# Kernel tuning notes

Measured on AMD Instinct MI355X. Metric: run time of the kernel, lower is better.

## Reference

```python
import jax, jax.numpy as jnp
import numpy as np

DIM = 1024; DEPTH = 6; HEADS = 16; DH = 64; NF = 16; VOCAB = 20000; B = 4; N = 1024
INNER = HEADS * DH
FF_INNER = int(DIM * 4 * 2 / 3)  # GEGLU inner dim = 2730


def _ln(x, g):
    # torch F.layer_norm with beta=0 buffer, eps=1e-5
    m = x.mean(-1, keepdims=True)
    v = ((x - m) ** 2).mean(-1, keepdims=True)
    return (x - m) / jnp.sqrt(v + 1e-5) * g


def _attn(x, ctx, mask, ln_g, Wq, Wkv, Wo):
    # faithful: LayerNorm applied to x (queries); context, if given, used raw for k/v
    xn = _ln(x, ln_g)
    kv_x = xn if ctx is None else ctx
    b, i, _ = x.shape
    j = kv_x.shape[1]
    q = (xn @ Wq).reshape(b, i, HEADS, DH) * (DH ** -0.5)
    k, v = jnp.split(kv_x @ Wkv, 2, axis=-1)
    k = k.reshape(b, j, HEADS, DH)
    v = v.reshape(b, j, HEADS, DH)
    sim = jnp.einsum('bihd,bjhd->bhij', q, k)
    sim = jnp.where(mask, sim, -jnp.finfo(sim.dtype).max)
    attn = jax.nn.softmax(sim, axis=-1)
    out = jnp.einsum('bhij,bjhd->bihd', attn, v).reshape(b, i, INNER)
    return out @ Wo


def _closs(a, b, ls):
    # CLIP-style ContrastiveLossWithTemperature
    an = a / jnp.linalg.norm(a, axis=-1, keepdims=True)
    bn = b / jnp.linalg.norm(b, axis=-1, keepdims=True)
    logits = jnp.exp(ls) * (an @ bn.T)
    lab = jnp.arange(a.shape[0])
    la = -jax.nn.log_softmax(logits, axis=-1)[lab, lab].mean()
    lb = -jax.nn.log_softmax(logits.T, axis=-1)[lab, lab].mean()
    return (la + lb) * 0.5


def setup_inputs() -> dict:
    key = jax.random.key(0)
    ks = jax.random.split(key, 16)
    rn = lambda k, s: jax.random.normal(k, s, jnp.float32) * 0.02
    return {
        'spliced_data': jax.random.normal(ks[0], (B, N), jnp.float32),
        'spliced_index': jax.random.randint(ks[1], (B, N), 0, VOCAB),
        'emb': rn(ks[2], (VOCAB, DIM)),
        'fusion_tokens': jax.random.normal(ks[3], (NF, DIM), jnp.float32),
        'return_tokens': jax.random.normal(ks[4], (2, DIM), jnp.float32),
        'ln1_g': jnp.ones((DEPTH, DIM), jnp.float32),
        'Wq': rn(ks[5], (DEPTH, DIM, INNER)),
        'Wkv': rn(ks[6], (DEPTH, DIM, 2 * INNER)),
        'Wo': rn(ks[7], (DEPTH, INNER, DIM)),
        'ln2_g': jnp.ones((DEPTH, DIM), jnp.float32),
        'Wff1': rn(ks[8], (DEPTH, DIM, 2 * FF_INNER)),
        'Wff2': rn(ks[9], (DEPTH, FF_INNER, DIM)),
        'norm_g': jnp.ones((DIM,), jnp.float32),
        'pool_ln_g': jnp.ones((DIM,), jnp.float32),
        'pWq': rn(ks[10], (DIM, INNER)),
        'pWkv': rn(ks[11], (DIM, 2 * INNER)),
        'pWo': rn(ks[12], (INNER, DIM)),
        'logit_scale_c': jnp.float32(np.log(1.0 / 0.07)),
        'logit_scale_f': jnp.float32(np.log(1.0 / 0.07)),
    }


def reference(spliced_data, spliced_index, emb, fusion_tokens, return_tokens,
              ln1_g, Wq, Wkv, Wo, ln2_g, Wff1, Wff2, norm_g,
              pool_ln_g, pWq, pWkv, pWo, logit_scale_c, logit_scale_f):
    b = spliced_data.shape[0]
    # BioZorroEncoder: value-weighted embedding lookup
    spliced_tokens = emb[spliced_index] * spliced_data[..., None]  # [b, N, DIM]
    tokens = jnp.concatenate(
        [spliced_tokens, jnp.broadcast_to(fusion_tokens, (b, NF, DIM))], axis=1)
    tt = jnp.concatenate([jnp.zeros((N,), jnp.int32), jnp.ones((NF,), jnp.int32)])
    # spliced attends spliced; fusion attends everything
    zmask = (tt[:, None] == tt[None, :]) | (tt[:, None] == 1)

    def body(t, p):
        l1, wq, wkv, wo, l2, w1, w2 = p
        t = _attn(t, None, zmask, l1, wq, wkv, wo) + t
        h = _ln(t, l2) @ w1
        xh, gate = jnp.split(h, 2, axis=-1)
        t = (jax.nn.gelu(gate, approximate=False) * xh) @ w2 + t
        return t, None

    tokens, _ = jax.lax.scan(body, tokens, (ln1_g, Wq, Wkv, Wo, ln2_g, Wff1, Wff2))
    tokens = _ln(tokens, norm_g)

    rtt = jnp.array([0, 1], jnp.int32)
    pm0 = rtt[:, None] == tt[None, :]
    # faithful to source operator precedence: (pm0 | rtt) == GLOBAL(2) -> all False
    pm = (pm0.astype(jnp.int32) | rtt[:, None]) == 2

    ret = jnp.broadcast_to(return_tokens, (b, 2, DIM))
    pooled = _attn(ret, tokens, pm, pool_ln_g, pWq, pWkv, pWo) + ret

    spliced = pooled[:, 0]
    fusion = pooled[:, 1]
    loss = _closs(spliced, spliced, logit_scale_c) + _closs(spliced, fusion, logit_scale_f)
    return loss
```

## Files before the change

### kernel.cpp

```cpp
#include <hip/hip_runtime.h>

typedef unsigned short u16;
typedef unsigned long long u64;
typedef __attribute__((ext_vector_type(8))) short short8;
typedef __attribute__((ext_vector_type(4))) float f32x4;

__device__ __forceinline__ u16 f2b(float f) {
  union { float f; unsigned u; } x; x.f = f;
  unsigned r = x.u + 0x7fffu + ((x.u >> 16) & 1u);
  return (u16)(r >> 16);
}
__device__ __forceinline__ float b2f(u16 h) {
  union { unsigned u; float f; } x; x.u = ((unsigned)h) << 16;
  return x.f;
}
__device__ __forceinline__ void gld16(const void* g, void* l) {
  __builtin_amdgcn_global_load_lds(
      (__attribute__((address_space(1))) const void*)g,
      (__attribute__((address_space(3))) void*)l, 16, 0, 0);
}

__global__ __launch_bounds__(256) void embed_k(
    const float* __restrict__ data, const int* __restrict__ idx,
    const float* __restrict__ emb, const float* __restrict__ fus,
    float* __restrict__ t) {
  int row = blockIdx.x;
  int b = row / 1040, n = row % 1040;
  int tid = threadIdx.x;
  const float4* src;
  float sc = 1.f;
  if (n < 1024) {
    int e = idx[b * 1024 + n];
    sc = data[b * 1024 + n];
    src = (const float4*)(emb + (long)e * 1024);
  } else {
    src = (const float4*)(fus + (long)(n - 1024) * 1024);
  }
  float4 v = src[tid];
  v.x *= sc; v.y *= sc; v.z *= sc; v.w *= sc;
  ((float4*)(t + (long)row * 1024))[tid] = v;
}

__global__ __launch_bounds__(256) void wtrans5_k(
    const float* __restrict__ sWq, const float* __restrict__ sWkv,
    const float* __restrict__ sWo, const float* __restrict__ sW1,
    const float* __restrict__ sW2,
    u16* __restrict__ dQkvT, u16* __restrict__ dWoT,
    u16* __restrict__ dF1T, u16* __restrict__ dF2T) {
  int id = blockIdx.x;
  const float* src; u16* dst; int K, N, Kpad, nx; float sc = 1.f;
  if (id < 1024)       { src = sWq;  dst = dQkvT;             K = 1024; N = 1024; Kpad = 1024; nx = 32; sc = 0.125f; }
  else if (id < 3072)  { id -= 1024; src = sWkv; dst = dQkvT + 1024 * 1024; K = 1024; N = 2048; Kpad = 1024; nx = 64; }
  else if (id < 4096)  { id -= 3072; src = sWo;  dst = dWoT;  K = 1024; N = 1024; Kpad = 1024; nx = 32; }
  else if (id < 9600)  { id -= 4096; src = sW1;  dst = dF1T;  K = 1024; N = 5460; Kpad = 1024; nx = 172; }
  else                 { id -= 9600; src = sW2;  dst = dF2T;  K = 2730; N = 1024; Kpad = 2752; nx = 32; }
  int n0 = (id % nx) * 32, k0 = (id / nx) * 32;
  __shared__ float tile[32][33];
  int x = threadIdx.x & 31, y = threadIdx.x >> 5;
#pragma unroll
  for (int i = 0; i < 4; i++) {
    int k = k0 + y + i * 8, n = n0 + x;
    tile[y + i * 8][x] = (k < K && n < N) ? src[(long)k * N + n] * sc : 0.f;
  }
  __syncthreads();
#pragma unroll
  for (int i = 0; i < 4; i++) {
    int n = n0 + y + i * 8, k = k0 + x;
    dst[(long)n * Kpad + k] = f2b(tile[x][y + i * 8]);
  }
}

__global__ __launch_bounds__(256) void ln_k(
    const float* __restrict__ t, const float* __restrict__ g,
    u16* __restrict__ xn) {
  int row = blockIdx.x, tid = threadIdx.x;
  int wave = tid >> 6, lane = tid & 63;
  float4 v = ((const float4*)(t + (long)row * 1024))[tid];
  float s = v.x + v.y + v.z + v.w;
#pragma unroll
  for (int o = 32; o > 0; o >>= 1) s += __shfl_xor(s, o, 64);
  __shared__ float r1[4], r2[4];
  if (lane == 0) r1[wave] = s;
  __syncthreads();
  float mean = (r1[0] + r1[1] + r1[2] + r1[3]) * (1.f / 1024.f);
  float dx = v.x - mean, dy = v.y - mean, dz = v.z - mean, dw = v.w - mean;
  float q = dx * dx + dy * dy + dz * dz + dw * dw;
#pragma unroll
  for (int o = 32; o > 0; o >>= 1) q += __shfl_xor(q, o, 64);
  if (lane == 0) r2[wave] = q;
  __syncthreads();
  float var = (r2[0] + r2[1] + r2[2] + r2[3]) * (1.f / 1024.f);
  float inv = rsqrtf(var + 1e-5f);
  float4 gv = ((const float4*)g)[tid];
  u64 pack = (u64)f2b(dx * inv * gv.x)
           | ((u64)f2b(dy * inv * gv.y) << 16)
           | ((u64)f2b(dz * inv * gv.z) << 32)
           | ((u64)f2b(dw * inv * gv.w) << 48);
  *(u64*)(xn + (long)row * 1024 + tid * 4) = pack;
}

__global__ __launch_bounds__(256) void lnred_k(
    float* __restrict__ t, const float* __restrict__ p0, const float* __restrict__ p1,
    const float* __restrict__ g, u16* __restrict__ xn) {
  int row = blockIdx.x, tid = threadIdx.x;
  int wave = tid >> 6, lane = tid & 63;
  long base = (long)row * 1024;
  float4 v = ((const float4*)(t + base))[tid];
  float4 a = ((const float4*)(p0 + base))[tid];
  float4 bq = ((const float4*)(p1 + base))[tid];
  v.x += a.x + bq.x; v.y += a.y + bq.y; v.z += a.z + bq.z; v.w += a.w + bq.w;
  ((float4*)(t + base))[tid] = v;
  float s = v.x + v.y + v.z + v.w;
#pragma unroll
  for (int o = 32; o > 0; o >>= 1) s += __shfl_xor(s, o, 64);
  __shared__ float r1[4], r2[4];
  if (lane == 0) r1[wave] = s;
  __syncthreads();
  float mean = (r1[0] + r1[1] + r1[2] + r1[3]) * (1.f / 1024.f);
  float dx = v.x - mean, dy = v.y - mean, dz = v.z - mean, dw = v.w - mean;
  float q = dx * dx + dy * dy + dz * dz + dw * dw;
#pragma unroll
  for (int o = 32; o > 0; o >>= 1) q += __shfl_xor(q, o, 64);
  if (lane == 0) r2[wave] = q;
  __syncthreads();
  float var = (r2[0] + r2[1] + r2[2] + r2[3]) * (1.f / 1024.f);
  float inv = rsqrtf(var + 1e-5f);
  float4 gv = ((const float4*)g)[tid];
  u64 pack = (u64)f2b(dx * inv * gv.x)
           | ((u64)f2b(dy * inv * gv.y) << 16)
           | ((u64)f2b(dz * inv * gv.z) << 32)
           | ((u64)f2b(dw * inv * gv.w) << 48);
  *(u64*)(xn + base + tid * 4) = pack;
}

__global__ __launch_bounds__(256) void redrow_k(
    float* __restrict__ t, const float* __restrict__ p0, const float* __restrict__ p1,
    float* __restrict__ rowm, float* __restrict__ rinv) {
  int row = blockIdx.x, tid = threadIdx.x;
  int wave = tid >> 6, lane = tid & 63;
  long base = (long)row * 1024;
  float4 v = ((const float4*)(t + base))[tid];
  float4 a = ((const float4*)(p0 + base))[tid];
  float4 bq = ((const float4*)(p1 + base))[tid];
  v.x += a.x + bq.x; v.y += a.y + bq.y; v.z += a.z + bq.z; v.w += a.w + bq.w;
  ((float4*)(t + base))[tid] = v;
  float s = v.x + v.y + v.z + v.w;
#pragma unroll
  for (int o = 32; o > 0; o >>= 1) s += __shfl_xor(s, o, 64);
  __shared__ float r1[4], r2[4];
  if (lane == 0) r1[wave] = s;
  __syncthreads();
  float mean = (r1[0] + r1[1] + r1[2] + r1[3]) * (1.f / 1024.f);
  float dx = v.x - mean, dy = v.y - mean, dz = v.z - mean, dw = v.w - mean;
  float q = dx * dx + dy * dy + dz * dz + dw * dw;
#pragma unroll
  for (int o = 32; o > 0; o >>= 1) q += __shfl_xor(q, o, 64);
  if (lane == 0) r2[wave] = q;
  __syncthreads();
  if (tid == 0) {
    float var = (r2[0] + r2[1] + r2[2] + r2[3]) * (1.f / 1024.f);
    rowm[row] = mean;
    rinv[row] = rsqrtf(var + 1e-5f);
  }
}

__global__ __launch_bounds__(256) void gemm_bt(
    const u16* __restrict__ A, int lda,
    const u16* __restrict__ Bt, int ldb,
    void* __restrict__ C, int ldc,
    int K, int mode, int gx, int ns, long pstride, u16* __restrict__ vt) {
  __shared__ u16 As[3][128 * 32];
  __shared__ u16 Bs[3][128 * 32];
  int tid = threadIdx.x;
  int wave = tid >> 6, lane = tid & 63;
  int col = lane & 15, grp = lane >> 4;
  int nwg = gridDim.x;
  int id = blockIdx.x;
  int q = nwg >> 3, r = nwg & 7;
  int xcd = id & 7, off = id >> 3;
  int wgid = (xcd < r ? xcd * (q + 1) : r * (q + 1) + (xcd - r) * q) + off;
  int tiles = nwg / ns;
  int ksp = wgid / tiles;
  int rem = wgid % tiles;
  int bm = rem % gx, bn = rem / gx;
  int nst = K >> 5;
  int k0 = ((nst * ksp) / ns) << 5;
  int k1 = ((nst * (ksp + 1)) / ns) << 5;
  int sr = wave * 16 + (lane >> 2);
  int sk = ((lane & 3) ^ ((lane >> 3) & 3)) * 8;
  const u16* aSrc = A + ((long)bm * 128 + sr) * lda + sk;
  const u16* bSrc = Bt + ((long)bn * 128 + sr) * ldb + sk;
  int wm = (wave >> 1) * 64, wn = (wave & 1) * 64;
  f32x4 acc[4][4] = {};

#define GSTAGE(buf, kt) do { \
    _Pragma("unroll") \
    for (int qq = 0; qq < 2; qq++) { \
      gld16(aSrc + (kt) + (long)qq * 64 * lda, &As[buf][wave * 512 + qq * 2048]); \
      gld16(bSrc + (kt) + (long)qq * 64 * ldb, &Bs[buf][wave * 512 + qq * 2048]); \
    } } while (0)

  GSTAGE(0, k0);
  if (k0 + 32 < k1) GSTAGE(1, k0 + 32);
  int cur = 0;
  int slot = (grp ^ ((col >> 1) & 3)) * 8;
  for (int kt = k0; kt < k1; kt += 32) {
    if (kt + 64 < k1) {
      int nb = cur + 2; if (nb >= 3) nb -= 3;
      GSTAGE(nb, kt + 64);
      asm volatile("s_waitcnt vmcnt(8)" ::: "memory");
    } else if (kt + 32 < k1) {
      asm volatile("s_waitcnt vmcnt(4)" ::: "memory");
    } else {
      asm volatile("s_waitcnt vmcnt(0)" ::: "memory");
    }
    __builtin_amdgcn_s_barrier();
    __builtin_amdgcn_sched_barrier(0);
    short8 af[4], bfv[4];
#pragma unroll
    for (int m = 0; m < 4; m++)
      af[m] = *(const short8*)&As[cur][(wm + m * 16 + col) * 32 + slot];
#pragma unroll
    for (int n = 0; n < 4; n++)
      bfv[n] = *(const short8*)&Bs[cur][(wn + n * 16 + col) * 32 + slot];
    __builtin_amdgcn_s_setprio(1);
#pragma unroll
    for (int m = 0; m < 4; m++)
#pragma unroll
      for (int n = 0; n < 4; n++)
        acc[m][n] = __builtin_amdgcn_mfma_f32_16x16x32_bf16(af[m], bfv[n], acc[m][n], 0, 0, 0);
    __builtin_amdgcn_s_setprio(0);
    __builtin_amdgcn_s_barrier();
    __builtin_amdgcn_sched_barrier(0);
    cur = (cur == 2) ? 0 : cur + 1;
  }
#undef GSTAGE
  long r0 = (long)bm * 128 + wm + grp * 4;
  int c0 = bn * 128 + wn + col;
  if (mode != 1) {
    u16* Cb = (u16*)C;
#pragma unroll
    for (int m = 0; m < 4; m++)
#pragma unroll
      for (int n = 0; n < 4; n++)
#pragma unroll
        for (int rr = 0; rr < 4; rr++)
          Cb[(r0 + m * 16 + rr) * ldc + c0 + n * 16] = f2b(acc[m][n][rr]);
    if (mode == 2 && bn >= 16) {
#pragma unroll
      for (int m = 0; m < 4; m++) {
        long row = r0 + m * 16;
        if (row < 4160) {
          int bidx = (int)(row / 1040);
          int j = (int)(row - (long)bidx * 1040);
#pragma unroll
          for (int n = 0; n < 4; n++) {
            int d = c0 + n * 16 - 2048;
            u64 pack = (u64)f2b(acc[m][n][0])
                     | ((u64)f2b(acc[m][n][1]) << 16)
                     | ((u64)f2b(acc[m][n][2]) << 32)
                     | ((u64)f2b(acc[m][n][3]) << 48);
            *(u64*)(vt + ((long)(bidx * 16 + (d >> 6)) * 64 + (d & 63)) * 1040 + j) = pack;
          }
        }
      }
    }
  } else {
    float* Cf = (float*)C + (long)ksp * pstride;
#pragma unroll
    for (int m = 0; m < 4; m++)
#pragma unroll
      for (int n = 0; n < 4; n++)
#pragma unroll
        for (int rr = 0; rr < 4; rr++)
          Cf[(r0 + m * 16 + rr) * ldc + c0 + n * 16] = acc[m][n][rr];
  }
}

__global__ __launch_bounds__(256) void attn_k(
    const u16* __restrict__ qkv, const u16* __restrict__ vt,
    u16* __restrict__ out) {
  int bh = blockIdx.x, it = blockIdx.y;
  int b = bh >> 4, h = bh & 15;
  int tid = threadIdx.x, wave = tid >> 6, lane = tid & 63;
  int col = lane & 15, grp = lane >> 4;
  int i0 = it * 64;
  int jmax = (it == 16) ? 1040 : 1024;
  const u16* qb = qkv + (long)b * 1040 * 3072 + h * 64;
  const u16* kb = qkv + (long)b * 1040 * 3072 + 1024 + h * 64;
  const u16* vb = vt + (long)bh * 64 * 1040;
  __shared__ u16 Ks[2][64 * 64];
  __shared__ u16 Vs[2][64 * 64];
  __shared__ u16 Ps[4][16 * 64];

  int srow0 = wave * 8 + (lane >> 3);
  int gsw = ((lane & 7) ^ (srow0 & 7)) * 8;
#define ASTAGE(buf, j0s) do { \
    int jv = (j0s) + gsw; if (jv >= 1040) jv = 1032; \
    _Pragma("unroll") \
    for (int qq = 0; qq < 2; qq++) { \
      int rr = qq * 32 + srow0; \
      gld16(kb + (long)((j0s) + rr) * 3072 + gsw, &Ks[buf][qq * 2048 + wave * 512]); \
      gld16(vb + (long)rr * 1040 + jv, &Vs[buf][qq * 2048 + wave * 512]); \
    } } while (0)

  short8 aq[2];
  int qrow = i0 + wave * 16;
#pragma unroll
  for (int kf = 0; kf < 2; kf++)
    aq[kf] = *(const short8*)(qb + (long)(qrow + col) * 3072 + kf * 32 + grp * 8);

  short8 one8 = {};
  if (col == 0) {
#pragma unroll
    for (int i = 0; i < 8; i++) one8[i] = (short)0x3F80;
  }

  f32x4 oa[4] = {};
  f32x4 oa1 = {};

  ASTAGE(0, 0);
  int cur = 0;
  for (int j0 = 0; j0 < jmax; j0 += 64) {
    if (j0 + 64 < jmax) {
      ASTAGE(cur ^ 1, j0 + 64);
      asm volatile("s_waitcnt vmcnt(4)" ::: "memory");
    } else {
      asm volatile("s_waitcnt vmcnt(0)" ::: "memory");
    }
    __builtin_amdgcn_s_barrier();
    __builtin_amdgcn_sched_barrier(0);
    f32x4 s[4] = {};
#pragma unroll
    for (int kf = 0; kf < 2; kf++) {
      short8 bk[4];
#pragma unroll
      for (int n = 0; n < 4; n++) {
        int rk = n * 16 + col;
        bk[n] = *(const short8*)&Ks[cur][rk * 64 + ((kf * 32 + grp * 8) ^ ((rk & 7) << 3))];
      }
      __builtin_amdgcn_s_setprio(1);
#pragma unroll
      for (int n = 0; n < 4; n++)
        s[n] = __builtin_amdgcn_mfma_f32_16x16x32_bf16(aq[kf], bk[n], s[n], 0, 0, 0);
      __builtin_amdgcn_s_setprio(0);
    }
    if (j0 + 64 > jmax) {
      int lim = jmax - j0;
#pragma unroll
      for (int n = 0; n < 4; n++) {
        if (n * 16 + col >= lim) {
#pragma unroll
          for (int r = 0; r < 4; r++) s[n][r] = -1e30f;
        }
      }
    }
#pragma unroll
    for (int r = 0; r < 4; r++) {
      int rp = grp * 4 + r;
#pragma unroll
      for (int n = 0; n < 4; n++) {
        float p = __expf(s[n][r]);
        Ps[wave][rp * 64 + ((n * 16 + col) ^ ((rp & 7) << 3))] = f2b(p);
      }
    }
#pragma unroll
    for (int kf = 0; kf < 2; kf++) {
      short8 ap, bv[4];
      int rm = col;
      ap = *(const short8*)&Ps[wave][rm * 64 + ((kf * 32 + grp * 8) ^ ((rm & 7) << 3))];
#pragma unroll
      for (int n = 0; n < 4; n++) {
        int rv = n * 16 + col;
        bv[n] = *(const short8*)&Vs[cur][rv * 64 + ((kf * 32 + grp * 8) ^ ((rv & 7) << 3))];
      }
      __builtin_amdgcn_s_setprio(1);
#pragma unroll
      for (int n = 0; n < 4; n++)
        oa[n] = __builtin_amdgcn_mfma_f32_16x16x32_bf16(ap, bv[n], oa[n], 0, 0, 0);
      oa1 = __builtin_amdgcn_mfma_f32_16x16x32_bf16(ap, one8, oa1, 0, 0, 0);
      __builtin_amdgcn_s_setprio(0);
    }
    __builtin_amdgcn_s_barrier();
    __builtin_amdgcn_sched_barrier(0);
    cur ^= 1;
  }
#undef ASTAGE
  float lr[4];
#pragma unroll
  for (int r = 0; r < 4; r++) lr[r] = __shfl(oa1[r], lane & 48, 64);
#pragma unroll
  for (int n = 0; n < 4; n++)
#pragma unroll
    for (int r = 0; r < 4; r++) {
      int i = i0 + wave * 16 + grp * 4 + r;
      if (i < 1040)
        out[((long)b * 1040 + i) * 1024 + h * 64 + n * 16 + col] = f2b(oa[n][r] / lr[r]);
    }
}

__global__ __launch_bounds__(256) void act_k(
    const u16* __restrict__ h, u16* __restrict__ act) {
  int row = blockIdx.x;
  int c = blockIdx.y * 1024 + threadIdx.x * 4;
  if (c >= 2752) return;
  const u16* hr = h + (long)row * 5504;
  u64 pack = 0;
#pragma unroll
  for (int i = 0; i < 4; i++) {
    int cc = c + i;
    float r = 0.f;
    if (cc < 2730) {
      float xh = b2f(hr[cc]);
      float gt = b2f(hr[2730 + cc]);
      float ge = 0.5f * gt * (1.f + erff(gt * 0.70710678118f));
      r = ge * xh;
    }
    pack |= ((u64)f2b(r)) << (16 * i);
  }
  *(u64*)(act + (long)row * 2752 + c) = pack;
}

__global__ __launch_bounds__(256) void wcolsum_k(
    const float* __restrict__ t, const float* __restrict__ rowm,
    const float* __restrict__ rinv, float* __restrict__ colsum,
    float* __restrict__ msum) {
  int b = blockIdx.x, c = blockIdx.y, tid = threadIdx.x;
  float a0 = 0, a1 = 0, a2 = 0, a3 = 0, ms = 0;
  for (int r = 0; r < 20; r++) {
    long row = (long)b * 1040 + c * 20 + r;
    float iv = rinv[row];
    float4 v = ((const float4*)(t + row * 1024))[tid];
    a0 += v.x * iv; a1 += v.y * iv; a2 += v.z * iv; a3 += v.w * iv;
    if (tid == 0) ms += rowm[row] * iv;
  }
  atomicAdd(&colsum[b * 1024 + tid * 4 + 0], a0);
  atomicAdd(&colsum[b * 1024 + tid * 4 + 1], a1);
  atomicAdd(&colsum[b * 1024 + tid * 4 + 2], a2);
  atomicAdd(&colsum[b * 1024 + tid * 4 + 3], a3);
  if (tid == 0) atomicAdd(&msum[b], ms);
}

__global__ __launch_bounds__(256) void mv1_k(
    const float* __restrict__ colsum, const float* __restrict__ msum,
    const float* __restrict__ g, const float* __restrict__ pWkv,
    float* __restrict__ tmp) {
  int b = blockIdx.x, n = blockIdx.y * 256 + threadIdx.x;
  float msb = msum[b];
  float acc = 0.f;
  for (int k = 0; k < 1024; k++) {
    float mk = g[k] * (colsum[b * 1024 + k] - msb);
    acc += mk * pWkv[(long)k * 2048 + 1024 + n];
  }
  tmp[b * 1024 + n] = acc * (1.f / 1040.f);
}

__global__ __launch_bounds__(256) void mv2_k(
    const float* __restrict__ tmp, const float* __restrict__ pWo,
    const float* __restrict__ ret, float* __restrict__ spl,
    float* __restrict__ fub) {
  int b = blockIdx.x, n = blockIdx.y * 256 + threadIdx.x;
  float acc = 0.f;
  for (int k = 0; k < 1024; k++) acc += tmp[b * 1024 + k] * pWo[(long)k * 1024 + n];
  spl[b * 1024 + n] = ret[n] + acc;
  fub[b * 1024 + n] = ret[1024 + n] + acc;
}

__device__ float closs_dev(const float L[4][4]) {
  float la = 0.f, lb = 0.f;
  for (int i = 0; i < 4; i++) {
    float mx = fmaxf(fmaxf(L[i][0], L[i][1]), fmaxf(L[i][2], L[i][3]));
    float sm = expf(L[i][0] - mx) + expf(L[i][1] - mx) + expf(L[i][2] - mx) + expf(L[i][3] - mx);
    la += mx + logf(sm) - L[i][i];
  }
  for (int j = 0; j < 4; j++) {
    float mx = fmaxf(fmaxf(L[0][j], L[1][j]), fmaxf(L[2][j], L[3][j]));
    float sm = expf(L[0][j] - mx) + expf(L[1][j] - mx) + expf(L[2][j] - mx) + expf(L[3][j] - mx);
    lb += mx + logf(sm) - L[j][j];
  }
  return 0.125f * (la + lb);
}

__global__ __launch_bounds__(256) void loss_k(
    const float* __restrict__ s, const float* __restrict__ f,
    const float* __restrict__ lsc, const float* __restrict__ lsf,
    float* __restrict__ out) {
  __shared__ float dots[36];
  int tid = threadIdx.x, wave = tid >> 6, lane = tid & 63;
  for (int d = wave; d < 36; d += 4) {
    const float *a, *bb;
    if (d < 16) { a = s + (d >> 2) * 1024; bb = s + (d & 3) * 1024; }
    else if (d < 32) { int e = d - 16; a = s + (e >> 2) * 1024; bb = f + (e & 3) * 1024; }
    else { a = f + (d - 32) * 1024; bb = a; }
    float p = 0.f;
    for (int k = lane; k < 1024; k += 64) p += a[k] * bb[k];
#pragma unroll
    for (int o = 32; o > 0; o >>= 1) p += __shfl_xor(p, o, 64);
    if (lane == 0) dots[d] = p;
  }
  __syncthreads();
  if (tid == 0) {
    float nS[4], nF[4];
    for (int i = 0; i < 4; i++) { nS[i] = sqrtf(dots[i * 4 + i]); nF[i] = sqrtf(dots[32 + i]); }
    float e1 = expf(lsc[0]), e2 = expf(lsf[0]);
    float L1[4][4], L2[4][4];
    for (int i = 0; i < 4; i++)
      for (int j = 0; j < 4; j++) {
        L1[i][j] = e1 * dots[i * 4 + j] / (nS[i] * nS[j]);
        L2[i][j] = e2 * dots[16 + i * 4 + j] / (nS[i] * nF[j]);
      }
    out[0] = closs_dev(L1) + closs_dev(L2);
  }
}

extern "C" void kernel_launch(void* const* d_in, const int* in_sizes, int n_in,
                              void* d_out, int out_size, void* d_ws, size_t ws_size,
                              hipStream_t stream) {
  (void)in_sizes; (void)n_in; (void)out_size; (void)ws_size;
  const float* sdata = (const float*)d_in[0];
  const int*   sidx  = (const int*)d_in[1];
  const float* emb   = (const float*)d_in[2];
  const float* fus   = (const float*)d_in[3];
  const float* ret   = (const float*)d_in[4];
  const float* ln1g  = (const float*)d_in[5];
  const float* Wq    = (const float*)d_in[6];
  const float* Wkv   = (const float*)d_in[7];
  const float* Wo    = (const float*)d_in[8];
  const float* ln2g  = (const float*)d_in[9];
  const float* Wff1  = (const float*)d_in[10];
  const float* Wff2  = (const float*)d_in[11];
  const float* normg = (const float*)d_in[12];
  const float* pWkv  = (const float*)d_in[15];
  const float* pWo   = (const float*)d_in[16];
  const float* lsc   = (const float*)d_in[17];
  const float* lsf   = (const float*)d_in[18];

  char* ws = (char*)d_ws;
  float* t   = (float*)(ws + 0L);
  u16* xn    = (u16*)(ws + 17301504L);
  char* U    = ws + 25952256L;
  u16* qkv   = (u16*)(U);
  u16* vtb   = (u16*)(U + 26738688L);
  u16* aout  = (u16*)(U + 35270656L);
  u16* hb    = (u16*)(U);
  u16* ab    = (u16*)(U + 46497792L);
  float* par0 = (float*)(U);
  float* par1 = (float*)(U + 17301504L);
  char* WT   = ws + 95698944L;
  u16* qkvT  = (u16*)(WT);
  u16* WoT   = (u16*)(WT + 6291456L);
  u16* f1T   = (u16*)(WT + 8388608L);
  u16* f2T   = (u16*)(WT + 19660800L);
  char* FIN  = ws + 120995840L;
  float* rowm   = (float*)(FIN);
  float* rinvp  = (float*)(FIN + 16640L);
  float* colsum = (float*)(FIN + 33280L);
  float* msum   = (float*)(FIN + 49664L);
  float* tmp    = (float*)(FIN + 49728L);
  float* spl    = (float*)(FIN + 66112L);
  float* fub    = (float*)(FIN + 82496L);
  const long PSTR = 4224L * 1024;

  embed_k<<<4160, 256, 0, stream>>>(sdata, sidx, emb, fus, t);

  for (int l = 0; l < 6; l++) {
    wtrans5_k<<<12352, 256, 0, stream>>>(
        Wq + (long)l * 1024 * 1024, Wkv + (long)l * 1024 * 2048,
        Wo + (long)l * 1024 * 1024, Wff1 + (long)l * 1024 * 5460,
        Wff2 + (long)l * 2730 * 1024, qkvT, WoT, f1T, f2T);

    if (l == 0)
      ln_k<<<4160, 256, 0, stream>>>(t, ln1g, xn);
    else
      lnred_k<<<4160, 256, 0, stream>>>(t, par0, par1, ln1g + l * 1024, xn);

    gemm_bt<<<33 * 24, 256, 0, stream>>>(xn, 1024, qkvT, 1024, qkv, 3072, 1024, 2, 33, 1, 0, vtb);
    attn_k<<<dim3(64, 17), 256, 0, stream>>>(qkv, vtb, aout);
    gemm_bt<<<33 * 8 * 2, 256, 0, stream>>>(aout, 1024, WoT, 1024, par0, 1024, 1024, 1, 33, 2, PSTR, vtb);
    lnred_k<<<4160, 256, 0, stream>>>(t, par0, par1, ln2g + l * 1024, xn);
    gemm_bt<<<33 * 43, 256, 0, stream>>>(xn, 1024, f1T, 1024, hb, 5504, 1024, 0, 33, 1, 0, vtb);
    act_k<<<dim3(4160, 3), 256, 0, stream>>>(hb, ab);
    gemm_bt<<<33 * 8 * 2, 256, 0, stream>>>(ab, 2752, f2T, 2752, par0, 1024, 2752, 1, 33, 2, PSTR, vtb);
  }

  redrow_k<<<4160, 256, 0, stream>>>(t, par0, par1, rowm, rinvp);
  hipMemsetAsync(colsum, 0, 16448, stream);
  wcolsum_k<<<dim3(4, 52), 256, 0, stream>>>(t, rowm, rinvp, colsum, msum);
  mv1_k<<<dim3(4, 4), 256, 0, stream>>>(colsum, msum, normg, pWkv, tmp);
  mv2_k<<<dim3(4, 4), 256, 0, stream>>>(tmp, pWo, ret, spl, fub);
  loss_k<<<1, 256, 0, stream>>>(spl, fub, lsc, lsf, (float*)d_out);
}
```

Measured before the change: 1.993 ms.

## Batch weight transposes into one launch, store split-K partials as bf16, vectorize act loads

Measured after the change: 3.246 ms. 62.9% more time.

```diff
diff --git a/kernel.cpp b/kernel.cpp
--- a/kernel.cpp
+++ b/kernel.cpp
@@ -41,19 +41,20 @@
   ((float4*)(t + (long)row * 1024))[tid] = v;
 }
 
-__global__ __launch_bounds__(256) void wtrans5_k(
+__global__ __launch_bounds__(256) void wtrans6_k(
     const float* __restrict__ sWq, const float* __restrict__ sWkv,
     const float* __restrict__ sWo, const float* __restrict__ sW1,
-    const float* __restrict__ sW2,
-    u16* __restrict__ dQkvT, u16* __restrict__ dWoT,
-    u16* __restrict__ dF1T, u16* __restrict__ dF2T) {
-  int id = blockIdx.x;
+    const float* __restrict__ sW2, u16* __restrict__ wt6) {
+  int gid = blockIdx.x;
+  int l = gid / 12352;
+  int id = gid - l * 12352;
+  u16* base = wt6 + (long)l * 12648448;
   const float* src; u16* dst; int K, N, Kpad, nx; float sc = 1.f;
-  if (id < 1024)       { src = sWq;  dst = dQkvT;             K = 1024; N = 1024; Kpad = 1024; nx = 32; sc = 0.125f; }
-  else if (id < 3072)  { id -= 1024; src = sWkv; dst = dQkvT + 1024 * 1024; K = 1024; N = 2048; Kpad = 1024; nx = 64; }
-  else if (id < 4096)  { id -= 3072; src = sWo;  dst = dWoT;  K = 1024; N = 1024; Kpad = 1024; nx = 32; }
-  else if (id < 9600)  { id -= 4096; src = sW1;  dst = dF1T;  K = 1024; N = 5460; Kpad = 1024; nx = 172; }
-  else                 { id -= 9600; src = sW2;  dst = dF2T;  K = 2730; N = 1024; Kpad = 2752; nx = 32; }
+  if (id < 1024)       { src = sWq  + (long)l * 1048576; dst = base;           K = 1024; N = 1024; Kpad = 1024; nx = 32; sc = 0.125f; }
+  else if (id < 3072)  { id -= 1024; src = sWkv + (long)l * 2097152; dst = base + 1048576; K = 1024; N = 2048; Kpad = 1024; nx = 64; }
+  else if (id < 4096)  { id -= 3072; src = sWo  + (long)l * 1048576; dst = base + 3145728; K = 1024; N = 1024; Kpad = 1024; nx = 32; }
+  else if (id < 9600)  { id -= 4096; src = sW1  + (long)l * 5591040; dst = base + 4194304; K = 1024; N = 5460; Kpad = 1024; nx = 172; }
+  else                 { id -= 9600; src = sW2  + (long)l * 2795520; dst = base + 9830400; K = 2730; N = 1024; Kpad = 2752; nx = 32; }
   int n0 = (id % nx) * 32, k0 = (id / nx) * 32;
   __shared__ float tile[32][33];
   int x = threadIdx.x & 31, y = threadIdx.x >> 5;
@@ -100,15 +101,18 @@
 }
 
 __global__ __launch_bounds__(256) void lnred_k(
-    float* __restrict__ t, const float* __restrict__ p0, const float* __restrict__ p1,
+    float* __restrict__ t, const u16* __restrict__ par, long pstr,
     const float* __restrict__ g, u16* __restrict__ xn) {
   int row = blockIdx.x, tid = threadIdx.x;
   int wave = tid >> 6, lane = tid & 63;
   long base = (long)row * 1024;
   float4 v = ((const float4*)(t + base))[tid];
-  float4 a = ((const float4*)(p0 + base))[tid];
-  float4 bq = ((const float4*)(p1 + base))[tid];
-  v.x += a.x + bq.x; v.y += a.y + bq.y; v.z += a.z + bq.z; v.w += a.w + bq.w;
+  u64 a0 = *(const u64*)(par + base + tid * 4);
+  u64 a1 = *(const u64*)(par + pstr + base + tid * 4);
+  v.x += b2f((u16)a0) + b2f((u16)a1);
+  v.y += b2f((u16)(a0 >> 16)) + b2f((u16)(a1 >> 16));
+  v.z += b2f((u16)(a0 >> 32)) + b2f((u16)(a1 >> 32));
+  v.w += b2f((u16)(a0 >> 48)) + b2f((u16)(a1 >> 48));
   ((float4*)(t + base))[tid] = v;
   float s = v.x + v.y + v.z + v.w;
 #pragma unroll
@@ -134,15 +138,18 @@
 }
 
 __global__ __launch_bounds__(256) void redrow_k(
-    float* __restrict__ t, const float* __restrict__ p0, const float* __restrict__ p1,
+    float* __restrict__ t, const u16* __restrict__ par, long pstr,
     float* __restrict__ rowm, float* __restrict__ rinv) {
   int row = blockIdx.x, tid = threadIdx.x;
   int wave = tid >> 6, lane = tid & 63;
   long base = (long)row * 1024;
   float4 v = ((const float4*)(t + base))[tid];
-  float4 a = ((const float4*)(p0 + base))[tid];
-  float4 bq = ((const float4*)(p1 + base))[tid];
-  v.x += a.x + bq.x; v.y += a.y + bq.y; v.z += a.z + bq.z; v.w += a.w + bq.w;
+  u64 a0 = *(const u64*)(par + base + tid * 4);
+  u64 a1 = *(const u64*)(par + pstr + base + tid * 4);
+  v.x += b2f((u16)a0) + b2f((u16)a1);
+  v.y += b2f((u16)(a0 >> 16)) + b2f((u16)(a1 >> 16));
+  v.z += b2f((u16)(a0 >> 32)) + b2f((u16)(a1 >> 32));
+  v.w += b2f((u16)(a0 >> 48)) + b2f((u16)(a1 >> 48));
   ((float4*)(t + base))[tid] = v;
   float s = v.x + v.y + v.z + v.w;
 #pragma unroll
@@ -266,14 +273,14 @@
       }
     }
   } else {
-    float* Cf = (float*)C + (long)ksp * pstride;
+    u16* Cf = (u16*)C + (long)ksp * pstride;
 #pragma unroll
     for (int m = 0; m < 4; m++)
 #pragma unroll
       for (int n = 0; n < 4; n++)
 #pragma unroll
         for (int rr = 0; rr < 4; rr++)
-          Cf[(r0 + m * 16 + rr) * ldc + c0 + n * 16] = acc[m][n][rr];
+          Cf[(r0 + m * 16 + rr) * ldc + c0 + n * 16] = f2b(acc[m][n][rr]);
   }
 }
 
@@ -405,14 +412,18 @@
   int c = blockIdx.y * 1024 + threadIdx.x * 4;
   if (c >= 2752) return;
   const u16* hr = h + (long)row * 5504;
+  u64 xh4 = *(const u64*)(hr + c);
+  unsigned g0 = *(const unsigned*)(hr + 2730 + c);
+  unsigned g1 = *(const unsigned*)(hr + 2732 + c);
+  u16 gv[4] = { (u16)g0, (u16)(g0 >> 16), (u16)g1, (u16)(g1 >> 16) };
   u64 pack = 0;
 #pragma unroll
   for (int i = 0; i < 4; i++) {
     int cc = c + i;
     float r = 0.f;
     if (cc < 2730) {
-      float xh = b2f(hr[cc]);
-      float gt = b2f(hr[2730 + cc]);
+      float xh = b2f((u16)(xh4 >> (16 * i)));
+      float gt = b2f(gv[i]);
       float ge = 0.5f * gt * (1.f + erff(gt * 0.70710678118f));
       r = ge * xh;
     }
@@ -544,13 +555,7 @@
   u16* aout  = (u16*)(U + 35270656L);
   u16* hb    = (u16*)(U);
   u16* ab    = (u16*)(U + 46497792L);
-  float* par0 = (float*)(U);
-  float* par1 = (float*)(U + 17301504L);
-  char* WT   = ws + 95698944L;
-  u16* qkvT  = (u16*)(WT);
-  u16* WoT   = (u16*)(WT + 6291456L);
-  u16* f1T   = (u16*)(WT + 8388608L);
-  u16* f2T   = (u16*)(WT + 19660800L);
+  u16* par   = (u16*)(U);
   char* FIN  = ws + 120995840L;
   float* rowm   = (float*)(FIN);
   float* rinvp  = (float*)(FIN + 16640L);
@@ -559,31 +564,34 @@
   float* tmp    = (float*)(FIN + 49728L);
   float* spl    = (float*)(FIN + 66112L);
   float* fub    = (float*)(FIN + 82496L);
+  u16* wt6   = (u16*)(ws + 300000000L);
   const long PSTR = 4224L * 1024;
 
   embed_k<<<4160, 256, 0, stream>>>(sdata, sidx, emb, fus, t);
+  wtrans6_k<<<6 * 12352, 256, 0, stream>>>(Wq, Wkv, Wo, Wff1, Wff2, wt6);
 
   for (int l = 0; l < 6; l++) {
-    wtrans5_k<<<12352, 256, 0, stream>>>(
-        Wq + (long)l * 1024 * 1024, Wkv + (long)l * 1024 * 2048,
-        Wo + (long)l * 1024 * 1024, Wff1 + (long)l * 1024 * 5460,
-        Wff2 + (long)l * 2730 * 1024, qkvT, WoT, f1T, f2T);
+    char* WL = (char*)wt6 + (long)l * 25296896;
+    u16* qkvT = (u16*)(WL);
+    u16* WoT  = (u16*)(WL + 6291456L);
+    u16* f1T  = (u16*)(WL + 8388608L);
+    u16* f2T  = (u16*)(WL + 19660800L);
 
     if (l == 0)
       ln_k<<<4160, 256, 0, stream>>>(t, ln1g, xn);
     else
-      lnred_k<<<4160, 256, 0, stream>>>(t, par0, par1, ln1g + l * 1024, xn);
+      lnred_k<<<4160, 256, 0, stream>>>(t, par, PSTR, ln1g + l * 1024, xn);
 
     gemm_bt<<<33 * 24, 256, 0, stream>>>(xn, 1024, qkvT, 1024, qkv, 3072, 1024, 2, 33, 1, 0, vtb);
     attn_k<<<dim3(64, 17), 256, 0, stream>>>(qkv, vtb, aout);
-    gemm_bt<<<33 * 8 * 2, 256, 0, stream>>>(aout, 1024, WoT, 1024, par0, 1024, 1024, 1, 33, 2, PSTR, vtb);
-    lnred_k<<<4160, 256, 0, stream>>>(t, par0, par1, ln2g + l * 1024, xn);
+    gemm_bt<<<33 * 8 * 2, 256, 0, stream>>>(aout, 1024, WoT, 1024, par, 1024, 1024, 1, 33, 2, PSTR, vtb);
+    lnred_k<<<4160, 256, 0, stream>>>(t, par, PSTR, ln2g + l * 1024, xn);
     gemm_bt<<<33 * 43, 256, 0, stream>>>(xn, 1024, f1T, 1024, hb, 5504, 1024, 0, 33, 1, 0, vtb);
     act_k<<<dim3(4160, 3), 256, 0, stream>>>(hb, ab);
-    gemm_bt<<<33 * 8 * 2, 256, 0, stream>>>(ab, 2752, f2T, 2752, par0, 1024, 2752, 1, 33, 2, PSTR, vtb);
-  }
-
-  redrow_k<<<4160, 256, 0, stream>>>(t, par0, par1, rowm, rinvp);
+    gemm_bt<<<33 * 8 * 2, 256, 0, stream>>>(ab, 2752, f2T, 2752, par, 1024, 2752, 1, 33, 2, PSTR, vtb);
+  }
+
+  redrow_k<<<4160, 256, 0, stream>>>(t, par, PSTR, rowm, rinvp);
   hipMemsetAsync(colsum, 0, 16448, stream);
   wcolsum_k<<<dim3(4, 52), 256, 0, stream>>>(t, rowm, rinvp, colsum, msum);
   mv1_k<<<dim3(4, 4), 256, 0, stream>>>(colsum, msum, normg, pWkv, tmp);
```
